# Performance work log

Hardware: AMD Instinct MI355X
Metric: run time of the kernel (lower is better)

## Reference

```python
import jax, jax.numpy as jnp
import numpy as np

H = 1024      # hidden_size
I = 2 * H     # intermediate_size (expand_factor=2)
N = 16        # ssm_state_size
K = 4         # conv_kernel
BATCH = 2
SEQ = 2048


def setup_inputs() -> dict:
    key = jax.random.key(0)
    k = jax.random.split(key, 6)
    x = jax.random.normal(k[0], (BATCH, SEQ, H), dtype=jnp.float32)
    # nn.Linear default init ~ U(-1/sqrt(fan_in), 1/sqrt(fan_in)); scale is fine for a reference
    W_in = jax.random.normal(k[1], (2 * I, H), dtype=jnp.float32) / np.sqrt(H)
    conv_w = jax.random.normal(k[2], (I, 1, K), dtype=jnp.float32) / np.sqrt(K)
    W_x = jax.random.normal(k[3], (2 * N + 1, I), dtype=jnp.float32) / np.sqrt(I)
    A_log = jax.random.normal(k[4], (I, N), dtype=jnp.float32)
    D = jnp.ones((I,), dtype=jnp.float32)
    W_out = jax.random.normal(k[5], (H, I), dtype=jnp.float32) / np.sqrt(I)
    return {"x": x, "W_in": W_in, "conv_w": conv_w, "W_x": W_x,
            "A_log": A_log, "D": D, "W_out": W_out}


def reference(x, W_in, conv_w, W_x, A_log, D, W_out):
    xz = jnp.einsum('bsh,ih->bsi', x, W_in)
    xp, z = jnp.split(xz, 2, axis=-1)
    # depthwise causal conv1d: pad left K-1 (torch pads both sides then slices [:S])
    xc = jax.lax.conv_general_dilated(
        xp.transpose(0, 2, 1),           # (B, I, S)
        conv_w,                          # (I, 1, K) = OIH with groups=I
        window_strides=(1,),
        padding=[(K - 1, 0)],
        feature_group_count=I,
        dimension_numbers=('NCH', 'OIH', 'NCH'),
    ).transpose(0, 2, 1)                 # (B, S, I)
    xc = jax.nn.silu(xc)
    # x_proj -> delta (1), B (N), C (N)
    xproj = jnp.einsum('bsi,pi->bsp', xc, W_x)   # (B,S,2N+1)
    delta = jax.nn.softplus(xproj[..., :1])       # (B,S,1)
    Bmat = xproj[..., 1:1 + N]                    # (B,S,N)
    Cmat = xproj[..., 1 + N:]                     # (B,S,N)
    A = -jnp.exp(A_log)                           # (I,N)
    # decay/states broadcast-reduce: (B,S,I,N) intermediates reduced over N
    decay = jnp.exp(delta[..., None] * A[None, None])            # (B,S,I,N)
    states = xc[..., None] * Bmat[:, :, None, :] * decay          # (B,S,I,N)
    y = jnp.sum(states * Cmat[:, :, None, :], axis=-1)            # (B,S,I)
    y = y + xc * D[None, None, :]
    return jnp.einsum('bsi,hi->bsh', y * jax.nn.silu(z), W_out)
```

## Files before the change

### kernel.cpp

```cpp
#include <hip/hip_runtime.h>

#define LOG2E 1.4426950408889634f

__device__ __forceinline__ float b2f(unsigned short u) {
    unsigned int v = ((unsigned int)u) << 16;
    return __builtin_bit_cast(float, v);
}
__device__ __forceinline__ unsigned short f2b(float f) {
    unsigned int u = __builtin_bit_cast(unsigned int, f);
    u += 0x7fffu + ((u >> 16) & 1u);
    return (unsigned short)(u >> 16);
}
__device__ __forceinline__ float fexp(float x) {
    return __builtin_amdgcn_exp2f(x * LOG2E);
}
__device__ __forceinline__ float silu_f(float x) {
    return x * __builtin_amdgcn_rcpf(1.0f + fexp(-x));
}
__device__ __forceinline__ unsigned short u4get(ushort4 v, int c) {
    return c == 0 ? v.x : c == 1 ? v.y : c == 2 ? v.z : v.w;
}

typedef const __attribute__((address_space(1))) unsigned int* gas_t;
typedef __attribute__((address_space(3))) unsigned int* las_t;
__device__ __forceinline__ void gl2lds16(const unsigned short* g, unsigned short* l) {
    __builtin_amdgcn_global_load_lds((gas_t)(const void*)g, (las_t)(void*)l, 16, 0, 0);
}

__global__ __launch_bounds__(256) void cvt_all_k(const float* __restrict__ x,
                                                 const float* __restrict__ W_in,
                                                 const float* __restrict__ W_out,
                                                 const float* __restrict__ W_x,
                                                 const float* __restrict__ Alog,
                                                 unsigned short* __restrict__ xb,
                                                 unsigned short* __restrict__ wib,
                                                 unsigned short* __restrict__ wob,
                                                 unsigned short* __restrict__ wxb,
                                                 float* __restrict__ A2) {
    int b = blockIdx.x;
    if (b >= 10306) {
        int i = (b - 10306) * 256 + threadIdx.x;
        float4 v = ((const float4*)Alog)[i];
        ((float4*)A2)[i] = make_float4(-fexp(v.x) * LOG2E, -fexp(v.y) * LOG2E,
                                       -fexp(v.z) * LOG2E, -fexp(v.w) * LOG2E);
        return;
    }
    const float* src;
    unsigned short* dst;
    if (b < 4096)       { src = x;     dst = xb;  }
    else if (b < 8192)  { src = W_in;  dst = wib; b -= 4096; }
    else if (b < 10240) { src = W_out; dst = wob; b -= 8192; }
    else                { src = W_x;   dst = wxb; b -= 10240; }
    int i = b * 256 + threadIdx.x;
    float4 v = ((const float4*)src)[i];
    *(ushort4*)(dst + (size_t)i * 4) = make_ushort4(f2b(v.x), f2b(v.y), f2b(v.z), f2b(v.w));
}

typedef __bf16 bf16x8 __attribute__((ext_vector_type(8)));
typedef float  fx4    __attribute__((ext_vector_type(4)));
typedef int    ix4    __attribute__((ext_vector_type(4)));
union FragU { ix4 i; bf16x8 b; };

template <bool OUT_BF16>
__global__ __launch_bounds__(256) void gemm_bt(const unsigned short* __restrict__ A,
                                               const unsigned short* __restrict__ B,
                                               void* __restrict__ C, int N, int K) {
    __shared__ __align__(16) unsigned short sA[128 * 64];
    __shared__ __align__(16) unsigned short sB[128 * 64];
    const int tid  = threadIdx.x;
    const int lane = tid & 63, wave = tid >> 6;
    const int bm = blockIdx.y * 128, bn = blockIdx.x * 128;
    const int wm = (wave >> 1) * 64, wn = (wave & 1) * 64;
    const int row16 = lane & 15, quad = lane >> 4;
    const int srow = lane >> 3;
    const int sc16 = (lane & 7) ^ srow;
    const unsigned short* gA = A + (size_t)(bm + wave * 32 + srow) * K + sc16 * 8;
    const unsigned short* gB = B + (size_t)(bn + wave * 32 + srow) * K + sc16 * 8;
    unsigned short* lA = sA + (wave * 4) * 512;
    unsigned short* lB = sB + (wave * 4) * 512;
    fx4 acc[4][4] = {};

    for (int kt = 0; kt < K; kt += 64) {
#pragma unroll
        for (int it = 0; it < 4; ++it) {
            gl2lds16(gA + (size_t)it * 8 * K + kt, lA + it * 512);
            gl2lds16(gB + (size_t)it * 8 * K + kt, lB + it * 512);
        }
        __syncthreads();
#pragma unroll
        for (int kk = 0; kk < 64; kk += 32) {
            FragU af[4], bf[4];
#pragma unroll
            for (int t = 0; t < 4; ++t) {
                int ra = wm + t * 16 + row16;
                af[t].i = *(const ix4*)(sA + ra * 64 + ((quad + (kk >> 3)) ^ (ra & 7)) * 8);
            }
#pragma unroll
            for (int t = 0; t < 4; ++t) {
                int rb = wn + t * 16 + row16;
                bf[t].i = *(const ix4*)(sB + rb * 64 + ((quad + (kk >> 3)) ^ (rb & 7)) * 8);
            }
#pragma unroll
            for (int tm = 0; tm < 4; ++tm)
#pragma unroll
                for (int tn = 0; tn < 4; ++tn)
                    acc[tm][tn] = __builtin_amdgcn_mfma_f32_16x16x32_bf16(
                        af[tm].b, bf[tn].b, acc[tm][tn], 0, 0, 0);
        }
        __syncthreads();
    }
#pragma unroll
    for (int tm = 0; tm < 4; ++tm) {
        int row0 = bm + wm + tm * 16 + quad * 4;
#pragma unroll
        for (int tn = 0; tn < 4; ++tn) {
            int col = bn + wn + tn * 16 + row16;
#pragma unroll
            for (int r = 0; r < 4; ++r) {
                float v = acc[tm][tn][r];
                if (OUT_BF16)
                    ((unsigned short*)C)[(size_t)(row0 + r) * N + col] = f2b(v);
                else
                    ((float*)C)[(size_t)(row0 + r) * N + col] = v;
            }
        }
    }
}

__global__ __launch_bounds__(256) void gemm_bt_n64(const unsigned short* __restrict__ A,
                                                   const unsigned short* __restrict__ B,
                                                   float* __restrict__ C, int N, int K) {
    __shared__ __align__(16) unsigned short sA[128 * 64];
    __shared__ __align__(16) unsigned short sB[64 * 64];
    const int tid  = threadIdx.x;
    const int lane = tid & 63, wave = tid >> 6;
    const int bm = blockIdx.y * 128, bn = blockIdx.x * 64;
    const int wm = wave * 32;
    const int row16 = lane & 15, quad = lane >> 4;
    const int srow = lane >> 3;
    const int sc16 = (lane & 7) ^ srow;
    const unsigned short* gA = A + (size_t)(bm + wave * 32 + srow) * K + sc16 * 8;
    const unsigned short* gB = B + (size_t)(bn + wave * 16 + srow) * K + sc16 * 8;
    unsigned short* lA = sA + (wave * 4) * 512;
    unsigned short* lB = sB + (wave * 2) * 512;
    fx4 acc[2][4] = {};

    for (int kt = 0; kt < K; kt += 64) {
#pragma unroll
        for (int it = 0; it < 4; ++it)
            gl2lds16(gA + (size_t)it * 8 * K + kt, lA + it * 512);
#pragma unroll
        for (int it = 0; it < 2; ++it)
            gl2lds16(gB + (size_t)it * 8 * K + kt, lB + it * 512);
        __syncthreads();
#pragma unroll
        for (int kk = 0; kk < 64; kk += 32) {
            FragU af[2], bf[4];
#pragma unroll
            for (int t = 0; t < 2; ++t) {
                int ra = wm + t * 16 + row16;
                af[t].i = *(const ix4*)(sA + ra * 64 + ((quad + (kk >> 3)) ^ (ra & 7)) * 8);
            }
#pragma unroll
            for (int t = 0; t < 4; ++t) {
                int rb = t * 16 + row16;
                bf[t].i = *(const ix4*)(sB + rb * 64 + ((quad + (kk >> 3)) ^ (rb & 7)) * 8);
            }
#pragma unroll
            for (int tm = 0; tm < 2; ++tm)
#pragma unroll
                for (int tn = 0; tn < 4; ++tn)
                    acc[tm][tn] = __builtin_amdgcn_mfma_f32_16x16x32_bf16(
                        af[tm].b, bf[tn].b, acc[tm][tn], 0, 0, 0);
        }
        __syncthreads();
    }
#pragma unroll
    for (int tm = 0; tm < 2; ++tm) {
        int row0 = bm + wm + tm * 16 + quad * 4;
#pragma unroll
        for (int tn = 0; tn < 4; ++tn) {
            int col = bn + tn * 16 + row16;
#pragma unroll
            for (int r = 0; r < 4; ++r)
                C[(size_t)(row0 + r) * N + col] = acc[tm][tn][r];
        }
    }
}

__global__ __launch_bounds__(256) void conv_xproj_k(const unsigned short* __restrict__ xz,
                                                    const float* __restrict__ cw,
                                                    const unsigned short* __restrict__ wxb,
                                                    float* __restrict__ dg) {
    __shared__ __align__(16) unsigned short sxc[8 * 2048];
    __shared__ float sX[4][16][49];
    const int tid  = threadIdx.x;
    const int lane = tid & 63, wave = tid >> 6;
    const int row16 = lane & 15, quad = lane >> 4;
    const int m0 = blockIdx.x * 8, s0 = m0 & 2047;

    {
        ushort4 ua[11], ub[11];
#pragma unroll
        for (int t = 0; t < 11; ++t) {
            int mr = (s0 - 3 + t >= 0) ? (m0 - 3 + t) : m0;
            const unsigned short* p = xz + (size_t)mr * 4096 + tid * 8;
            ua[t] = *(const ushort4*)p;
            ub[t] = *(const ushort4*)(p + 4);
        }
        float w[8][4];
        const float4* cw4 = (const float4*)cw;
#pragma unroll
        for (int c = 0; c < 8; ++c) {
            float4 t4 = cw4[tid * 8 + c];
            w[c][0] = t4.x; w[c][1] = t4.y; w[c][2] = t4.z; w[c][3] = t4.w;
        }
#pragma unroll
        for (int t = 0; t < 3; ++t)
            if (s0 - 3 + t < 0) { ua[t] = make_ushort4(0, 0, 0, 0); ub[t] = make_ushort4(0, 0, 0, 0); }
#pragma unroll
        for (int j = 0; j < 8; ++j) {
            float acc[8] = {0, 0, 0, 0, 0, 0, 0, 0};
#pragma unroll
            for (int k = 0; k < 4; ++k) {
                ushort4 a = ua[j + k], b = ub[j + k];
                float v[8] = {b2f(a.x), b2f(a.y), b2f(a.z), b2f(a.w),
                              b2f(b.x), b2f(b.y), b2f(b.z), b2f(b.w)};
#pragma unroll
                for (int c = 0; c < 8; ++c) acc[c] += v[c] * w[c][k];
            }
            unsigned short* q = sxc + j * 2048 + ((tid ^ (j & 7)) * 8);
            *(ushort4*)q       = make_ushort4(f2b(silu_f(acc[0])), f2b(silu_f(acc[1])),
                                              f2b(silu_f(acc[2])), f2b(silu_f(acc[3])));
            *(ushort4*)(q + 4) = make_ushort4(f2b(silu_f(acc[4])), f2b(silu_f(acc[5])),
                                              f2b(silu_f(acc[6])), f2b(silu_f(acc[7])));
        }
    }
    __syncthreads();

    {
        fx4 acc[3] = {};
        const unsigned short* bp = wxb + (size_t)row16 * 2048 + wave * 512 + quad * 8;
        const int arow = row16 & 7;
        const int cbase = wave * 64 + quad;
#pragma unroll 4
        for (int kk = 0; kk < 512; kk += 32) {
            FragU a, b0, b1, b2;
            int c16 = cbase + (kk >> 3);
            a.i  = *(const ix4*)(sxc + arow * 2048 + ((c16 ^ arow) * 8));
            b0.i = *(const ix4*)(bp + kk);
            b1.i = *(const ix4*)(bp + 16 * 2048 + kk);
            b2.i = *(const ix4*)(bp + 32 * 2048 + kk);
            acc[0] = __builtin_amdgcn_mfma_f32_16x16x32_bf16(a.b, b0.b, acc[0], 0, 0, 0);
            acc[1] = __builtin_amdgcn_mfma_f32_16x16x32_bf16(a.b, b1.b, acc[1], 0, 0, 0);
            acc[2] = __builtin_amdgcn_mfma_f32_16x16x32_bf16(a.b, b2.b, acc[2], 0, 0, 0);
        }
#pragma unroll
        for (int t = 0; t < 3; ++t)
#pragma unroll
            for (int r = 0; r < 4; ++r)
                sX[wave][quad * 4 + r][t * 16 + row16] = acc[t][r];
    }
    __syncthreads();
    for (int idx = tid; idx < 136; idx += 256) {
        int rr = idx / 17, q = idx - rr * 17;
        float o;
        if (q == 0) {
            float v = sX[0][rr][0] + sX[1][rr][0] + sX[2][rr][0] + sX[3][rr][0];
            o = (v > 20.f) ? v : log1pf(fexp(v));
        } else {
            float bs = sX[0][rr][q]      + sX[1][rr][q]      + sX[2][rr][q]      + sX[3][rr][q];
            float cs = sX[0][rr][q + 16] + sX[1][rr][q + 16] + sX[2][rr][q + 16] + sX[3][rr][q + 16];
            o = bs * cs;
        }
        dg[(size_t)(m0 + rr) * 17 + q] = o;
    }
}

__global__ __launch_bounds__(256, 2) void conv_ssm_k(const unsigned short* __restrict__ xz,
                                                     const float* __restrict__ cw,
                                                     const float* __restrict__ dg,
                                                     const float* __restrict__ A2,
                                                     const float* __restrict__ Dv,
                                                     unsigned short* __restrict__ y2) {
    __shared__ float sdg[8 * 17];
    const int tid = threadIdx.x;
    const int m0 = blockIdx.y * 8, s0 = m0 & 2047;
    const int ch0 = blockIdx.x * 1024 + tid * 4;
    if (tid < 136) sdg[tid] = dg[(size_t)m0 * 17 + tid];

    ushort4 uw[11];
#pragma unroll
    for (int t = 0; t < 11; ++t) {
        int mr = (s0 - 3 + t >= 0) ? (m0 - 3 + t) : m0;
        uw[t] = *(const ushort4*)(xz + (size_t)mr * 4096 + ch0);
    }
    ushort4 zu[8];
#pragma unroll
    for (int j = 0; j < 8; ++j)
        zu[j] = *(const ushort4*)(xz + (size_t)(m0 + j) * 4096 + 2048 + ch0);
    float w[4][4];
    const float4* cw4 = (const float4*)cw;
#pragma unroll
    for (int c = 0; c < 4; ++c) {
        float4 t4 = cw4[ch0 + c];
        w[c][0] = t4.x; w[c][1] = t4.y; w[c][2] = t4.z; w[c][3] = t4.w;
    }
    float a2[4][16];
#pragma unroll
    for (int c = 0; c < 4; ++c) {
        const float4* ar = (const float4*)(A2 + (size_t)(ch0 + c) * 16);
#pragma unroll
        for (int n4 = 0; n4 < 4; ++n4) {
            float4 t4 = ar[n4];
            a2[c][n4 * 4 + 0] = t4.x; a2[c][n4 * 4 + 1] = t4.y;
            a2[c][n4 * 4 + 2] = t4.z; a2[c][n4 * 4 + 3] = t4.w;
        }
    }
    float4 dvv = *(const float4*)(Dv + ch0);
    float dv[4] = {dvv.x, dvv.y, dvv.z, dvv.w};
#pragma unroll
    for (int t = 0; t < 3; ++t)
        if (s0 - 3 + t < 0) uw[t] = make_ushort4(0, 0, 0, 0);
    __syncthreads();

#pragma unroll
    for (int j = 0; j < 8; ++j) {
        float delta = sdg[j * 17];
        float Gr[16];
#pragma unroll
        for (int n = 0; n < 16; ++n) Gr[n] = sdg[j * 17 + 1 + n];
        unsigned short ov[4];
#pragma unroll
        for (int c = 0; c < 4; ++c) {
            float acc = 0.f;
#pragma unroll
            for (int k = 0; k < 4; ++k)
                acc += b2f(u4get(uw[j + k], c)) * w[c][k];
            float xc = silu_f(acc);
            float ssum = 0.f;
#pragma unroll
            for (int n = 0; n < 16; ++n)
                ssum += Gr[n] * __builtin_amdgcn_exp2f(delta * a2[c][n]);
            float y = xc * (dv[c] + ssum);
            ov[c] = f2b(y * silu_f(b2f(u4get(zu[j], c))));
        }
        *(ushort4*)(y2 + (size_t)(m0 + j) * 2048 + ch0) = make_ushort4(ov[0], ov[1], ov[2], ov[3]);
    }
}

extern "C" void kernel_launch(void* const* d_in, const int* in_sizes, int n_in,
                              void* d_out, int out_size, void* d_ws, size_t ws_size,
                              hipStream_t stream) {
    const float* x      = (const float*)d_in[0];
    const float* W_in   = (const float*)d_in[1];
    const float* conv_w = (const float*)d_in[2];
    const float* W_x    = (const float*)d_in[3];
    const float* A_log  = (const float*)d_in[4];
    const float* Dvec   = (const float*)d_in[5];
    const float* W_out  = (const float*)d_in[6];

    char* ws = (char*)d_ws;
    unsigned short* xb  = (unsigned short*)(ws);
    unsigned short* wib = (unsigned short*)(ws + 8388608);
    unsigned short* wob = (unsigned short*)(ws + 16777216);
    unsigned short* xz  = (unsigned short*)(ws + 20971520);
    unsigned short* y2  = (unsigned short*)(ws + 54525952);
    unsigned short* wxb = (unsigned short*)(ws + 71303168);
    float*          dgp = (float*)        (ws + 71499776);
    float*          a2p = (float*)        (ws + 71778304);

    cvt_all_k<<<10338, 256, 0, stream>>>(x, W_in, W_out, W_x, A_log, xb, wib, wob, wxb, a2p);
    gemm_bt<true><<<dim3(32, 32), 256, 0, stream>>>(xb, wib, xz, 4096, 1024);
    conv_xproj_k<<<512, 256, 0, stream>>>(xz, conv_w, wxb, dgp);
    conv_ssm_k<<<dim3(2, 512), 256, 0, stream>>>(xz, conv_w, dgp, a2p, Dvec, y2);
    gemm_bt_n64<<<dim3(16, 32), 256, 0, stream>>>(y2, wob, (float*)d_out, 1024, 2048);
}
```

Measured before the change: 215.5 us.

## Overlap weight casts with first GEMM and shrink output GEMM tiles

The conversions of W_out, W_x and A_log move out of the standalone cast kernel and into extra leading blocks of the first GEMM launch, so they run alongside GEMM tiles instead of before them. The cast kernel now handles only x and W_in, which the first GEMM needs. The output projection GEMM changes from 128x64 to 64x64 tiles, doubling the block count to 1024 for better CU occupancy, at the cost of less data reuse per block.

```diff
diff --git a/kernel.cpp b/kernel.cpp
--- a/kernel.cpp
+++ b/kernel.cpp
@@ -27,49 +27,57 @@
     __builtin_amdgcn_global_load_lds((gas_t)(const void*)g, (las_t)(void*)l, 16, 0, 0);
 }
 
-__global__ __launch_bounds__(256) void cvt_all_k(const float* __restrict__ x,
-                                                 const float* __restrict__ W_in,
-                                                 const float* __restrict__ W_out,
-                                                 const float* __restrict__ W_x,
-                                                 const float* __restrict__ Alog,
-                                                 unsigned short* __restrict__ xb,
-                                                 unsigned short* __restrict__ wib,
-                                                 unsigned short* __restrict__ wob,
-                                                 unsigned short* __restrict__ wxb,
-                                                 float* __restrict__ A2) {
-    int b = blockIdx.x;
-    if (b >= 10306) {
-        int i = (b - 10306) * 256 + threadIdx.x;
-        float4 v = ((const float4*)Alog)[i];
-        ((float4*)A2)[i] = make_float4(-fexp(v.x) * LOG2E, -fexp(v.y) * LOG2E,
-                                       -fexp(v.z) * LOG2E, -fexp(v.w) * LOG2E);
-        return;
-    }
-    const float* src;
-    unsigned short* dst;
-    if (b < 4096)       { src = x;     dst = xb;  }
-    else if (b < 8192)  { src = W_in;  dst = wib; b -= 4096; }
-    else if (b < 10240) { src = W_out; dst = wob; b -= 8192; }
-    else                { src = W_x;   dst = wxb; b -= 10240; }
-    int i = b * 256 + threadIdx.x;
-    float4 v = ((const float4*)src)[i];
-    *(ushort4*)(dst + (size_t)i * 4) = make_ushort4(f2b(v.x), f2b(v.y), f2b(v.z), f2b(v.w));
-}
-
 typedef __bf16 bf16x8 __attribute__((ext_vector_type(8)));
 typedef float  fx4    __attribute__((ext_vector_type(4)));
 typedef int    ix4    __attribute__((ext_vector_type(4)));
 union FragU { ix4 i; bf16x8 b; };
 
-template <bool OUT_BF16>
-__global__ __launch_bounds__(256) void gemm_bt(const unsigned short* __restrict__ A,
-                                               const unsigned short* __restrict__ B,
-                                               void* __restrict__ C, int N, int K) {
+__global__ __launch_bounds__(256) void cast_xw_k(const float* __restrict__ x,
+                                                 const float* __restrict__ W_in,
+                                                 unsigned short* __restrict__ xb,
+                                                 unsigned short* __restrict__ wib) {
+    int b = blockIdx.x;
+    const float* src = (b < 4096) ? x : W_in;
+    unsigned short* dst = (b < 4096) ? xb : wib;
+    int i = (b & 4095) * 256 + threadIdx.x;
+    float4 v = ((const float4*)src)[i];
+    *(ushort4*)(dst + (size_t)i * 4) = make_ushort4(f2b(v.x), f2b(v.y), f2b(v.z), f2b(v.w));
+}
+
+__global__ __launch_bounds__(256) void gemm1_cast_k(const unsigned short* __restrict__ A,
+                                                    const unsigned short* __restrict__ B,
+                                                    unsigned short* __restrict__ C,
+                                                    const float* __restrict__ W_out,
+                                                    const float* __restrict__ W_x,
+                                                    const float* __restrict__ Alog,
+                                                    unsigned short* __restrict__ wob,
+                                                    unsigned short* __restrict__ wxb,
+                                                    float* __restrict__ A2) {
+    const int bid = blockIdx.x;
+    if (bid < 2146) {
+        if (bid < 2048) {
+            int i = bid * 256 + threadIdx.x;
+            float4 v = ((const float4*)W_out)[i];
+            *(ushort4*)(wob + (size_t)i * 4) = make_ushort4(f2b(v.x), f2b(v.y), f2b(v.z), f2b(v.w));
+        } else if (bid < 2114) {
+            int i = (bid - 2048) * 256 + threadIdx.x;
+            float4 v = ((const float4*)W_x)[i];
+            *(ushort4*)(wxb + (size_t)i * 4) = make_ushort4(f2b(v.x), f2b(v.y), f2b(v.z), f2b(v.w));
+        } else {
+            int i = (bid - 2114) * 256 + threadIdx.x;
+            float4 v = ((const float4*)Alog)[i];
+            ((float4*)A2)[i] = make_float4(-fexp(v.x) * LOG2E, -fexp(v.y) * LOG2E,
+                                           -fexp(v.z) * LOG2E, -fexp(v.w) * LOG2E);
+        }
+        return;
+    }
+    const int g = bid - 2146;
+    const int N = 4096, K = 1024;
     __shared__ __align__(16) unsigned short sA[128 * 64];
     __shared__ __align__(16) unsigned short sB[128 * 64];
     const int tid  = threadIdx.x;
     const int lane = tid & 63, wave = tid >> 6;
-    const int bm = blockIdx.y * 128, bn = blockIdx.x * 128;
+    const int bm = (g >> 5) * 128, bn = (g & 31) * 128;
     const int wm = (wave >> 1) * 64, wn = (wave & 1) * 64;
     const int row16 = lane & 15, quad = lane >> 4;
     const int srow = lane >> 3;
@@ -116,75 +124,60 @@
         for (int tn = 0; tn < 4; ++tn) {
             int col = bn + wn + tn * 16 + row16;
 #pragma unroll
-            for (int r = 0; r < 4; ++r) {
-                float v = acc[tm][tn][r];
-                if (OUT_BF16)
-                    ((unsigned short*)C)[(size_t)(row0 + r) * N + col] = f2b(v);
-                else
-                    ((float*)C)[(size_t)(row0 + r) * N + col] = v;
-            }
-        }
-    }
-}
-
-__global__ __launch_bounds__(256) void gemm_bt_n64(const unsigned short* __restrict__ A,
-                                                   const unsigned short* __restrict__ B,
-                                                   float* __restrict__ C, int N, int K) {
-    __shared__ __align__(16) unsigned short sA[128 * 64];
+            for (int r = 0; r < 4; ++r)
+                C[(size_t)(row0 + r) * N + col] = f2b(acc[tm][tn][r]);
+        }
+    }
+}
+
+__global__ __launch_bounds__(256) void gemm_bt_64(const unsigned short* __restrict__ A,
+                                                  const unsigned short* __restrict__ B,
+                                                  float* __restrict__ C, int N, int K) {
+    __shared__ __align__(16) unsigned short sA[64 * 64];
     __shared__ __align__(16) unsigned short sB[64 * 64];
     const int tid  = threadIdx.x;
     const int lane = tid & 63, wave = tid >> 6;
-    const int bm = blockIdx.y * 128, bn = blockIdx.x * 64;
-    const int wm = wave * 32;
+    const int bm = blockIdx.y * 64, bn = blockIdx.x * 64;
+    const int wm = wave * 16;
     const int row16 = lane & 15, quad = lane >> 4;
     const int srow = lane >> 3;
     const int sc16 = (lane & 7) ^ srow;
-    const unsigned short* gA = A + (size_t)(bm + wave * 32 + srow) * K + sc16 * 8;
+    const unsigned short* gA = A + (size_t)(bm + wave * 16 + srow) * K + sc16 * 8;
     const unsigned short* gB = B + (size_t)(bn + wave * 16 + srow) * K + sc16 * 8;
-    unsigned short* lA = sA + (wave * 4) * 512;
+    unsigned short* lA = sA + (wave * 2) * 512;
     unsigned short* lB = sB + (wave * 2) * 512;
-    fx4 acc[2][4] = {};
+    fx4 acc[4] = {};
 
     for (int kt = 0; kt < K; kt += 64) {
 #pragma unroll
-        for (int it = 0; it < 4; ++it)
+        for (int it = 0; it < 2; ++it) {
             gl2lds16(gA + (size_t)it * 8 * K + kt, lA + it * 512);
-#pragma unroll
-        for (int it = 0; it < 2; ++it)
             gl2lds16(gB + (size_t)it * 8 * K + kt, lB + it * 512);
+        }
         __syncthreads();
 #pragma unroll
         for (int kk = 0; kk < 64; kk += 32) {
-            FragU af[2], bf[4];
-#pragma unroll
-            for (int t = 0; t < 2; ++t) {
-                int ra = wm + t * 16 + row16;
-                af[t].i = *(const ix4*)(sA + ra * 64 + ((quad + (kk >> 3)) ^ (ra & 7)) * 8);
-            }
+            FragU af, bf[4];
+            int ra = wm + row16;
+            af.i = *(const ix4*)(sA + ra * 64 + ((quad + (kk >> 3)) ^ (ra & 7)) * 8);
 #pragma unroll
             for (int t = 0; t < 4; ++t) {
                 int rb = t * 16 + row16;
                 bf[t].i = *(const ix4*)(sB + rb * 64 + ((quad + (kk >> 3)) ^ (rb & 7)) * 8);
             }
 #pragma unroll
-            for (int tm = 0; tm < 2; ++tm)
-#pragma unroll
-                for (int tn = 0; tn < 4; ++tn)
-                    acc[tm][tn] = __builtin_amdgcn_mfma_f32_16x16x32_bf16(
-                        af[tm].b, bf[tn].b, acc[tm][tn], 0, 0, 0);
+            for (int tn = 0; tn < 4; ++tn)
+                acc[tn] = __builtin_amdgcn_mfma_f32_16x16x32_bf16(af.b, bf[tn].b, acc[tn], 0, 0, 0);
         }
         __syncthreads();
     }
-#pragma unroll
-    for (int tm = 0; tm < 2; ++tm) {
-        int row0 = bm + wm + tm * 16 + quad * 4;
-#pragma unroll
-        for (int tn = 0; tn < 4; ++tn) {
-            int col = bn + tn * 16 + row16;
-#pragma unroll
-            for (int r = 0; r < 4; ++r)
-                C[(size_t)(row0 + r) * N + col] = acc[tm][tn][r];
-        }
+    const int row0 = bm + wm + quad * 4;
+#pragma unroll
+    for (int tn = 0; tn < 4; ++tn) {
+        int col = bn + tn * 16 + row16;
+#pragma unroll
+        for (int r = 0; r < 4; ++r)
+            C[(size_t)(row0 + r) * N + col] = acc[tn][r];
     }
 }
 
@@ -370,9 +363,9 @@
     float*          dgp = (float*)        (ws + 71499776);
     float*          a2p = (float*)        (ws + 71778304);
 
-    cvt_all_k<<<10338, 256, 0, stream>>>(x, W_in, W_out, W_x, A_log, xb, wib, wob, wxb, a2p);
-    gemm_bt<true><<<dim3(32, 32), 256, 0, stream>>>(xb, wib, xz, 4096, 1024);
+    cast_xw_k<<<8192, 256, 0, stream>>>(x, W_in, xb, wib);
+    gemm1_cast_k<<<3170, 256, 0, stream>>>(xb, wib, xz, W_out, W_x, A_log, wob, wxb, a2p);
     conv_xproj_k<<<512, 256, 0, stream>>>(xz, conv_w, wxb, dgp);
     conv_ssm_k<<<dim3(2, 512), 256, 0, stream>>>(xz, conv_w, dgp, a2p, Dvec, y2);
-    gemm_bt_n64<<<dim3(16, 32), 256, 0, stream>>>(y2, wob, (float*)d_out, 1024, 2048);
-}
+    gemm_bt_64<<<dim3(16, 64), 256, 0, stream>>>(y2, wob, (float*)d_out, 1024, 2048);
+}
```

Result: faster. 207.4 us (-3.7%).
